# Kernel tuning notes

Hardware: AMD Instinct MI355X
Metric: run time of the kernel (lower is better)

Reference implementation:

```python
import jax, jax.numpy as jnp
import numpy as np

H = 32        # num query heads
HKV = 8       # num kv heads
D = 128       # head_dim
SCALE = D ** -0.5
FP8_MAX = 448.0   # e4m3 max
EPS = 1e-8
PAGE = 256
NPAGES = 20
SQ = 1024     # new diffusion tokens
CTX = 3072    # cached context tokens
DIFF_BLK = 32 # diffusion block size


def setup_inputs() -> dict:
    key = jax.random.key(0)
    ks = jax.random.split(key, 6)
    q = jax.random.normal(ks[0], (SQ, H * D), dtype=jnp.float32)
    k = jax.random.normal(ks[1], (SQ, HKV * D), dtype=jnp.float32)
    v = jax.random.normal(ks[2], (SQ, HKV * D), dtype=jnp.float32)
    # paged caches (values already stored in quantized units)
    k_cache = jax.random.normal(ks[3], (NPAGES, PAGE, HKV, D), dtype=jnp.float32)
    v_cache = jax.random.normal(ks[4], (NPAGES, PAGE, HKV, D), dtype=jnp.float32)
    # new tokens go into slots right after the context
    slot_mapping = jnp.arange(CTX, CTX + SQ, dtype=jnp.int32)
    cache_slots = jnp.arange(CTX, dtype=jnp.int32)
    # diffusion mask: full visibility of context, block-causal among new tokens
    blk = jnp.arange(SQ) // DIFF_BLK
    ctx_mask = jnp.ones((SQ, CTX), dtype=bool)
    new_mask = blk[:, None] >= blk[None, :]
    block_mask = jnp.concatenate([ctx_mask, new_mask], axis=1)  # [SQ, CTX+SQ]
    return {"q": q, "k": k, "v": v, "k_cache": k_cache, "v_cache": v_cache,
            "slot_mapping": slot_mapping, "cache_slots": cache_slots,
            "block_mask": block_mask}


def reference(q, k, v, k_cache, v_cache, slot_mapping, cache_slots, block_mask):
    k3 = k.reshape(-1, HKV, D)
    v3 = v.reshape(-1, HKV, D)
    qh = q.reshape(-1, H, D)

    # ---- FP8 scale tracking: per-kv-head absmax over (token, dim) ----
    k_scale = jnp.maximum(jnp.max(jnp.abs(k3), axis=(0, 2)) / FP8_MAX, EPS)  # [HKV]
    v_scale = jnp.maximum(jnp.max(jnp.abs(v3), axis=(0, 2)) / FP8_MAX, EPS)

    # ---- paged KV-cache store with inline quantization ----
    kc = k_cache.reshape(-1, HKV, D)  # [NPAGES*PAGE, HKV, D]
    vc = v_cache.reshape(-1, HKV, D)
    k_q = jnp.clip(k3 / k_scale[None, :, None], -FP8_MAX, FP8_MAX)
    v_q = jnp.clip(v3 / v_scale[None, :, None], -FP8_MAX, FP8_MAX)
    kc = kc.at[slot_mapping].set(k_q)
    vc = vc.at[slot_mapping].set(v_q)

    # ---- load context tokens from cache and dequantize ----
    k_ctx = kc[cache_slots] * k_scale[None, :, None]  # [CTX, HKV, D]
    v_ctx = vc[cache_slots] * v_scale[None, :, None]
    k_comb = jnp.concatenate([k_ctx, k3], axis=0)  # [SKV, HKV, D]
    v_comb = jnp.concatenate([v_ctx, v3], axis=0)

    # ---- GQA flex attention with token-level block mask ----
    G = H // HKV
    k_g = jnp.repeat(k_comb, G, axis=1)  # [SKV, H, D]
    v_g = jnp.repeat(v_comb, G, axis=1)
    scores = jnp.einsum('qhd,khd->hqk', qh, k_g) * SCALE  # [H, SQ, SKV]
    scores = jnp.where(block_mask[None, :, :], scores, jnp.float32(-1e30))
    probs = jax.nn.softmax(scores, axis=-1)
    o = jnp.einsum('hqk,khd->qhd', probs, v_g)  # [SQ, H, D]
    return o.reshape(-1, H * D)
```

## Files before the change

kernel.cpp:

```cpp
#include <hip/hip_runtime.h>
#include <stdint.h>

#define H 32
#define HKV 8
#define D 128
#define SQ 1024
#define CTX 3072
#define SKV 4096
#define FP8_MAX_C 448.0f
#define EPS_C 1e-8f

typedef __attribute__((ext_vector_type(4))) float f32x4;
typedef __attribute__((ext_vector_type(8))) __bf16 bf16x8;
typedef __attribute__((ext_vector_type(8))) unsigned short u16x8;

__device__ __forceinline__ unsigned short f2bf(float x) {
  unsigned int u = __builtin_bit_cast(unsigned int, x);
  u += 0x7fffu + ((u >> 16) & 1u);
  return (unsigned short)(u >> 16);
}

__device__ __forceinline__ f32x4 mfma16(bf16x8 a, bf16x8 b, f32x4 c) {
  return __builtin_amdgcn_mfma_f32_16x16x32_bf16(a, b, c, 0, 0, 0);
}

__device__ __forceinline__ void gld16(const unsigned short* g, char* l) {
  __builtin_amdgcn_global_load_lds(
      (const __attribute__((address_space(1))) unsigned int*)g,
      (__attribute__((address_space(3))) unsigned int*)l, 16, 0, 0);
}

__device__ __forceinline__ void stage_sync() {
  asm volatile("s_waitcnt vmcnt(0)" ::: "memory");
  __builtin_amdgcn_sched_barrier(0);
  __syncthreads();
}

__global__ void scales_part(const float* __restrict__ k,
                            const float* __restrict__ v,
                            unsigned int* __restrict__ smax) {
  const int b = blockIdx.x & 15;
  const int part = blockIdx.x >> 4;
  const float* src = (b < HKV) ? k : v;
  const int h = b & 7;
  const int tid = threadIdx.x;
  const int d0 = (tid & 31) * 4;
  float mx = 0.f;
  const int t1 = part * 128 + 128;
  for (int t = part * 128 + (tid >> 5); t < t1; t += 8) {
    float4 vv = *reinterpret_cast<const float4*>(src + (size_t)t * (HKV * D) + h * D + d0);
    mx = fmaxf(mx, fmaxf(fmaxf(fabsf(vv.x), fabsf(vv.y)),
                         fmaxf(fabsf(vv.z), fabsf(vv.w))));
  }
  __shared__ float red[256];
  red[tid] = mx;
  __syncthreads();
  for (int s = 128; s > 0; s >>= 1) {
    if (tid < s) red[tid] = fmaxf(red[tid], red[tid + s]);
    __syncthreads();
  }
  if (tid == 0) atomicMax(&smax[b], __float_as_uint(red[0]));
}

__global__ void scales_fin(const unsigned int* __restrict__ smax,
                           float* __restrict__ scales) {
  const int i = threadIdx.x;
  if (i < 16) scales[i] = fmaxf(__uint_as_float(smax[i]) / FP8_MAX_C, EPS_C);
}

__global__ void prep_kv(const float* __restrict__ k,
                        const float* __restrict__ v,
                        const float* __restrict__ k_cache,
                        const float* __restrict__ v_cache,
                        const int* __restrict__ cache_slots,
                        const float* __restrict__ scales,
                        unsigned short* __restrict__ k_comb,
                        unsigned short* __restrict__ v_combT) {
  if (blockIdx.x < 2048) {
    const int tid = blockIdx.x * 256 + threadIdx.x;
    const int d8 = tid & 15;
    const int t = (tid >> 4) & (SKV - 1);
    const int h = tid >> 16;
    const int d0 = d8 * 8;
    const float* src;
    float mul;
    if (t < CTX) {
      int slot = cache_slots[t];
      src = k_cache + (size_t)slot * (HKV * D) + h * D + d0;
      mul = scales[h];
    } else {
      src = k + (size_t)(t - CTX) * (HKV * D) + h * D + d0;
      mul = 1.f;
    }
    float4 a = *reinterpret_cast<const float4*>(src);
    float4 bb = *reinterpret_cast<const float4*>(src + 4);
    u16x8 r;
    r[0] = f2bf(a.x * mul);  r[1] = f2bf(a.y * mul);
    r[2] = f2bf(a.z * mul);  r[3] = f2bf(a.w * mul);
    r[4] = f2bf(bb.x * mul); r[5] = f2bf(bb.y * mul);
    r[6] = f2bf(bb.z * mul); r[7] = f2bf(bb.w * mul);
    *reinterpret_cast<u16x8*>(k_comb + ((size_t)h * SKV + t) * D + d0) = r;
  } else {
    const int tid = (blockIdx.x - 2048) * 256 + threadIdx.x;
    const int d = tid & 127;
    const int t8 = (tid >> 7) & 511;
    const int h = tid >> 16;
    const int t0 = t8 * 8;
    const float sc = scales[8 + h];
    u16x8 r;
#pragma unroll
    for (int i = 0; i < 8; ++i) {
      int t = t0 + i;
      float val;
      if (t < CTX) {
        int slot = cache_slots[t];
        val = v_cache[(size_t)slot * (HKV * D) + h * D + d] * sc;
      } else {
        val = v[(size_t)(t - CTX) * (HKV * D) + h * D + d];
      }
      r[i] = f2bf(val);
    }
    *reinterpret_cast<u16x8*>(v_combT + ((size_t)h * D + d) * SKV + t0) = r;
  }
}

#define LDBF(p) (*reinterpret_cast<const bf16x8*>(p))
#define Z4 ((f32x4){0.f, 0.f, 0.f, 0.f})

#define EXP4(SREG, P, RSV)                                                     \
  {                                                                            \
    P[0] = __builtin_amdgcn_exp2f(SREG[0] - m);                                \
    P[1] = __builtin_amdgcn_exp2f(SREG[1] - m);                                \
    P[2] = __builtin_amdgcn_exp2f(SREG[2] - m);                                \
    P[3] = __builtin_amdgcn_exp2f(SREG[3] - m);                                \
    RSV += (P[0] + P[1]) + (P[2] + P[3]);                                      \
  }

#define CVTPK(DST, LO, HI)                                                     \
  asm("v_cvt_pk_bf16_f32 %0, %1, %2" : "=v"(DST) : "v"(LO), "v"(HI));
#define SW32(A, B)                                                             \
  asm("v_permlane32_swap_b32 %0, %1" : "+v"(A), "+v"(B));
#define SW16(A, B)                                                             \
  asm("v_permlane16_swap_b32 %0, %1" : "+v"(A), "+v"(B));

#define PTRANS32(P0, P1, PF)                                                   \
  {                                                                            \
    unsigned int A_, Ap_, B_, Bp_;                                             \
    CVTPK(A_, P0[0], P0[1]) CVTPK(Ap_, P0[2], P0[3])                           \
    CVTPK(B_, P1[0], P1[1]) CVTPK(Bp_, P1[2], P1[3])                           \
    SW32(A_, B_) SW16(A_, B_)                                                  \
    SW32(Ap_, Bp_) SW16(Ap_, Bp_)                                              \
    union { unsigned int d[4]; bf16x8 v; } u_;                                 \
    u_.d[0] = A_; u_.d[1] = Ap_; u_.d[2] = B_; u_.d[3] = Bp_;                  \
    PF = u_.v;                                                                 \
  }

#define QKSF(SF, SA, SB)                                                       \
  {                                                                            \
    bf16x8 a0 = LDBF(kc + SF * 4096 + kx0);                                    \
    bf16x8 a1 = LDBF(kc + SF * 4096 + kx1);                                    \
    bf16x8 a2 = LDBF(kc + SF * 4096 + kx2);                                    \
    bf16x8 a3 = LDBF(kc + SF * 4096 + kx3);                                    \
    SA = mfma16(a0, qa0, SA); SA = mfma16(a1, qa1, SA);                        \
    SA = mfma16(a2, qa2, SA); SA = mfma16(a3, qa3, SA);                        \
    SB = mfma16(a0, qb0, SB); SB = mfma16(a1, qb1, SB);                        \
    SB = mfma16(a2, qb2, SB); SB = mfma16(a3, qb3, SB);                        \
  }

#define QLOADS                                                                 \
  {                                                                            \
    const float qs = 0.088388347648318447f * 1.4426950408889634f;              \
    const float* qpA = q + (size_t)(qbase + lo) * (H * D) + hqa * D;           \
    const float* qpB = qpA + D;                                                \
    _Pragma("unroll")                                                          \
    for (int ks = 0; ks < 4; ++ks) {                                           \
      float4 a = *reinterpret_cast<const float4*>(qpA + ks * 32 + g * 8);      \
      float4 b = *reinterpret_cast<const float4*>(qpA + ks * 32 + g * 8 + 4);  \
      union { unsigned short u[8]; bf16x8 v; } f;                              \
      f.u[0] = f2bf(a.x * qs); f.u[1] = f2bf(a.y * qs);                        \
      f.u[2] = f2bf(a.z * qs); f.u[3] = f2bf(a.w * qs);                        \
      f.u[4] = f2bf(b.x * qs); f.u[5] = f2bf(b.y * qs);                        \
      f.u[6] = f2bf(b.z * qs); f.u[7] = f2bf(b.w * qs);                        \
      if (ks == 0) qa0 = f.v; else if (ks == 1) qa1 = f.v;                     \
      else if (ks == 2) qa2 = f.v; else qa3 = f.v;                             \
      a = *reinterpret_cast<const float4*>(qpB + ks * 32 + g * 8);             \
      b = *reinterpret_cast<const float4*>(qpB + ks * 32 + g * 8 + 4);         \
      f.u[0] = f2bf(a.x * qs); f.u[1] = f2bf(a.y * qs);                        \
      f.u[2] = f2bf(a.z * qs); f.u[3] = f2bf(a.w * qs);                        \
      f.u[4] = f2bf(b.x * qs); f.u[5] = f2bf(b.y * qs);                        \
      f.u[6] = f2bf(b.z * qs); f.u[7] = f2bf(b.w * qs);                        \
      if (ks == 0) qb0 = f.v; else if (ks == 1) qb1 = f.v;                     \
      else if (ks == 2) qb2 = f.v; else qb3 = f.v;                             \
    }                                                                          \
  }

#define EPILOGUE(DSTEXPR)                                                      \
  lsa += __shfl_xor(lsa, 16); lsa += __shfl_xor(lsa, 32);                      \
  lsb += __shfl_xor(lsb, 16); lsb += __shfl_xor(lsb, 32);                      \
  float* dst = (DSTEXPR);                                                      \
  if (g == 0) {                                                                \
    float2 v;                                                                  \
    v.x = m; v.y = lsa;                                                        \
    *reinterpret_cast<float2*>(ml + ((size_t)part * SQ * H + (qbase + lo) * H + hqa) * 2) = v; \
    v.y = lsb;                                                                 \
    *reinterpret_cast<float2*>(ml + ((size_t)part * SQ * H + (qbase + lo) * H + hqa + 1) * 2) = v; \
  }                                                                            \
  _Pragma("unroll")                                                            \
  for (int r = 0; r < 4; ++r) {                                                \
    float* opa = dst + (size_t)(qbase + g * 4 + r) * (H * D) + hqa * D + lo;   \
    float* opb = opa + D;                                                      \
    opa[0 * 16] = aa0[r]; opb[0 * 16] = ab0[r];                                \
    opa[1 * 16] = aa1[r]; opb[1 * 16] = ab1[r];                                \
    opa[2 * 16] = aa2[r]; opb[2 * 16] = ab2[r];                                \
    opa[3 * 16] = aa3[r]; opb[3 * 16] = ab3[r];                                \
    opa[4 * 16] = aa4[r]; opb[4 * 16] = ab4[r];                                \
    opa[5 * 16] = aa5[r]; opb[5 * 16] = ab5[r];                                \
    opa[6 * 16] = aa6[r]; opb[6 * 16] = ab6[r];                                \
    opa[7 * 16] = aa7[r]; opb[7 * 16] = ab7[r];                                \
  }

#define RESCALE_ALL                                                            \
  if (!__all(pmax - m <= 8.f)) {                                               \
    float rm = fmaxf(pmax, __shfl_xor(pmax, 16));                              \
    rm = fmaxf(rm, __shfl_xor(rm, 32));                                        \
    float mn = fmaxf(m, rm);                                                   \
    float scl = __builtin_amdgcn_exp2f(m - mn);                                \
    lsa *= scl; lsb *= scl;                                                    \
    aa0 *= scl; aa1 *= scl; aa2 *= scl; aa3 *= scl;                            \
    aa4 *= scl; aa5 *= scl; aa6 *= scl; aa7 *= scl;                            \
    ab0 *= scl; ab1 *= scl; ab2 *= scl; ab3 *= scl;                            \
    ab4 *= scl; ab5 *= scl; ab6 *= scl; ab7 *= scl;                            \
    m = mn;                                                                    \
  }

#define STAGE32(TB, BUFO)                                                      \
  {                                                                            \
    _Pragma("unroll")                                                          \
    for (int j = 0; j < 2; ++j) {                                              \
      const int c = j * 256 + tid;                                             \
      const int r_ = c >> 4;                                                   \
      const int lc_ = (c & 15) ^ (r_ & 7);                                     \
      gld16(kb + (size_t)((TB) + r_) * D + lc_ * 8,                            \
            smem + (BUFO) + c * 16);                                           \
      const int dv_ = c >> 2;                                                  \
      const int cv_ = (c & 3) ^ ((dv_ >> 1) & 3);                              \
      gld16(vb + (size_t)dv_ * SKV + (TB) + cv_ * 8,                           \
            smem + (BUFO) + 8192 + c * 16);                                    \
    }                                                                          \
  }

#define SOFTMAX32                                                              \
  float pmax = fmaxf(fmaxf(fmaxf(sa0[0], sa0[1]), fmaxf(sa0[2], sa0[3])),      \
                     fmaxf(fmaxf(sa1[0], sa1[1]), fmaxf(sa1[2], sa1[3])));     \
  pmax = fmaxf(pmax,                                                           \
               fmaxf(fmaxf(fmaxf(sb0[0], sb0[1]), fmaxf(sb0[2], sb0[3])),      \
                     fmaxf(fmaxf(sb1[0], sb1[1]), fmaxf(sb1[2], sb1[3]))));    \
  RESCALE_ALL                                                                  \
  float pa0[4], pa1[4], pb0[4], pb1[4];                                        \
  EXP4(sa0, pa0, lsa) EXP4(sa1, pa1, lsa)                                      \
  EXP4(sb0, pb0, lsb) EXP4(sb1, pb1, lsb)                                      \
  PTRANS32(pa0, pa1, pfa)                                                      \
  PTRANS32(pb0, pb1, pfb)

#define VLOAD                                                                  \
  vf0 = LDBF(vc + 0 * 1024 + vx); vf1 = LDBF(vc + 1 * 1024 + vx);              \
  vf2 = LDBF(vc + 2 * 1024 + vx); vf3 = LDBF(vc + 3 * 1024 + vx);              \
  vf4 = LDBF(vc + 4 * 1024 + vx); vf5 = LDBF(vc + 5 * 1024 + vx);              \
  vf6 = LDBF(vc + 6 * 1024 + vx); vf7 = LDBF(vc + 7 * 1024 + vx);

#define PVREG                                                                  \
  aa0 = mfma16(pfa_p, vf0, aa0); ab0 = mfma16(pfb_p, vf0, ab0);                \
  aa1 = mfma16(pfa_p, vf1, aa1); ab1 = mfma16(pfb_p, vf1, ab1);                \
  aa2 = mfma16(pfa_p, vf2, aa2); ab2 = mfma16(pfb_p, vf2, ab2);                \
  aa3 = mfma16(pfa_p, vf3, aa3); ab3 = mfma16(pfb_p, vf3, ab3);                \
  aa4 = mfma16(pfa_p, vf4, aa4); ab4 = mfma16(pfb_p, vf4, ab4);                \
  aa5 = mfma16(pfa_p, vf5, aa5); ab5 = mfma16(pfb_p, vf5, ab5);                \
  aa6 = mfma16(pfa_p, vf6, aa6); ab6 = mfma16(pfb_p, vf6, ab6);                \
  aa7 = mfma16(pfa_p, vf7, aa7); ab7 = mfma16(pfb_p, vf7, ab7);

__launch_bounds__(256, 2)
__global__ void attn_kernel(const float* __restrict__ q,
                            const unsigned short* __restrict__ k_comb,
                            const unsigned short* __restrict__ v_combT,
                            float* __restrict__ out,
                            float* __restrict__ parts,
                            float* __restrict__ ml) {
  extern __shared__ __align__(16) char smem[];
  const int bid = blockIdx.x;
  const int hkv = bid & 7;
  const int qp_raw = (bid >> 3) & 31;
  const int part = bid >> 8;
  const int qp = part ? (31 - qp_raw) : qp_raw;
  const int tid = threadIdx.x;
  const int wid = tid >> 6;
  const int l = tid & 63;
  const int lo = l & 15;
  const int g = l >> 4;
  const int qbase = qp * 32 + (wid >> 1) * 16;
  const int hqa = hkv * 4 + (wid & 1) * 2;
  const int n32 = 97 + qp;
  const int t0 = (part * n32) >> 1;
  const int t1 = ((part + 1) * n32) >> 1;

  const unsigned short* kb = k_comb + (size_t)hkv * SKV * D;
  const unsigned short* vb = v_combT + (size_t)hkv * D * SKV;

  bf16x8 qa0, qa1, qa2, qa3, qb0, qb1, qb2, qb3;
  QLOADS

  f32x4 aa0 = Z4, aa1 = Z4, aa2 = Z4, aa3 = Z4;
  f32x4 aa4 = Z4, aa5 = Z4, aa6 = Z4, aa7 = Z4;
  f32x4 ab0 = Z4, ab1 = Z4, ab2 = Z4, ab3 = Z4;
  f32x4 ab4 = Z4, ab5 = Z4, ab6 = Z4, ab7 = Z4;
  float m = -1e30f;
  float lsa = 0.f, lsb = 0.f;

  const int xr = lo & 7;
  const int kx0 = ((0 + g) ^ xr) << 4;
  const int kx1 = ((4 + g) ^ xr) << 4;
  const int kx2 = ((8 + g) ^ xr) << 4;
  const int kx3 = ((12 + g) ^ xr) << 4;
  const int vx = ((g ^ ((lo >> 1) & 3))) << 4;
  const char* kbl = smem + lo * 256;
  const char* vbl = smem + 8192 + lo * 64;

  bf16x8 pfa_p, pfb_p;
  bf16x8 vf0, vf1, vf2, vf3, vf4, vf5, vf6, vf7;

  int cur = 0;
  STAGE32(t0 * 32, 0)
  stage_sync();

  {
    if (t0 + 1 < t1) STAGE32((t0 + 1) * 32, 16384)
    const char* kc = kbl;
    const char* vc = vbl;
    f32x4 sa0 = Z4, sa1 = Z4, sb0 = Z4, sb1 = Z4;
    __builtin_amdgcn_s_setprio(1);
    QKSF(0, sa0, sb0)
    QKSF(1, sa1, sb1)
    __builtin_amdgcn_s_setprio(0);
    bf16x8 pfa, pfb;
    SOFTMAX32
    VLOAD
    pfa_p = pfa; pfb_p = pfb;
    stage_sync();
    cur = 1;
  }

  for (int t = t0 + 1; t < t1; ++t) {
    if (t + 1 < t1) STAGE32((t + 1) * 32, (cur ^ 1) * 16384)

    const char* kc = kbl + cur * 16384;
    const char* vc = vbl + cur * 16384;

    f32x4 sa0 = Z4, sa1 = Z4, sb0 = Z4, sb1 = Z4;
    __builtin_amdgcn_s_setprio(1);
    QKSF(0, sa0, sb0)
    QKSF(1, sa1, sb1)
    PVREG
    __builtin_amdgcn_s_setprio(0);

    bf16x8 pfa, pfb;
    SOFTMAX32
    VLOAD
    pfa_p = pfa; pfb_p = pfb;

    stage_sync();
    cur ^= 1;
  }

  PVREG

  EPILOGUE(part == 0 ? out : parts)
}

__global__ void merge_kernel(float* __restrict__ out,
                             const float* __restrict__ parts,
                             const float* __restrict__ ml) {
  const int idx = blockIdx.x * 256 + threadIdx.x;
  const int h = (idx >> 5) & 31;
  const int qrow = idx >> 10;
  const float2* mp = (const float2*)ml;
  float2 A = mp[qrow * H + h];
  float2 B = mp[SQ * H + qrow * H + h];
  float mm = fmaxf(A.x, B.x);
  float wa = __builtin_amdgcn_exp2f(A.x - mm);
  float wb = __builtin_amdgcn_exp2f(B.x - mm);
  float inv = 1.f / (A.y * wa + B.y * wb);
  float4 oa = reinterpret_cast<float4*>(out)[idx];
  float4 ob = reinterpret_cast<const float4*>(parts)[idx];
  float4 r;
  r.x = (oa.x * wa + ob.x * wb) * inv;
  r.y = (oa.y * wa + ob.y * wb) * inv;
  r.z = (oa.z * wa + ob.z * wb) * inv;
  r.w = (oa.w * wa + ob.w * wb) * inv;
  reinterpret_cast<float4*>(out)[idx] = r;
}

extern "C" void kernel_launch(void* const* d_in, const int* in_sizes, int n_in,
                              void* d_out, int out_size, void* d_ws, size_t ws_size,
                              hipStream_t stream) {
  (void)in_sizes; (void)n_in; (void)out_size; (void)ws_size;
  const float* q = (const float*)d_in[0];
  const float* k = (const float*)d_in[1];
  const float* v = (const float*)d_in[2];
  const float* k_cache = (const float*)d_in[3];
  const float* v_cache = (const float*)d_in[4];
  const int* cache_slots = (const int*)d_in[6];
  float* out = (float*)d_out;

  unsigned int* smax = (unsigned int*)d_ws;
  float* scales = (float*)((char*)d_ws + 64);
  unsigned short* k_comb = (unsigned short*)((char*)d_ws + 256);
  unsigned short* v_combT = k_comb + (size_t)HKV * SKV * D;
  float* parts = (float*)((char*)d_ws + 256 + (size_t)16 * 1024 * 1024);
  float* ml = parts + (size_t)SQ * H * D;

  hipMemsetAsync(smax, 0, 64, stream);
  scales_part<<<128, 256, 0, stream>>>(k, v, smax);
  scales_fin<<<1, 64, 0, stream>>>(smax, scales);
  prep_kv<<<4096, 256, 0, stream>>>(k, v, k_cache, v_cache, cache_slots,
                                    scales, k_comb, v_combT);
  attn_kernel<<<512, 256, 32768, stream>>>(q, k_comb, v_combT, out, parts, ml);
  merge_kernel<<<4096, 256, 0, stream>>>(out, parts, ml);
}
```

Before: 110.9 us.

## Fuse FP8 scale reduction into KV prep and apply dequant scales in attention

Removes the separate scale-reduction and scale-finalize kernels by computing per-head absmax inside prep_kv while it already reads the new K/V tokens. Because scales are not known during prep, context K/V are stored unscaled in bf16 and the attention kernel applies the K scale to the scores and the V scale to the probabilities for context tiles (t < 96). This saves two launches and a redundant pass over K/V, at the cost of extra multiplies in the softmax path. Storing unscaled context values in bf16 also changes rounding slightly.

```diff
diff --git a/kernel.cpp b/kernel.cpp
--- a/kernel.cpp
+++ b/kernel.cpp
@@ -36,46 +36,17 @@
   __syncthreads();
 }
 
-__global__ void scales_part(const float* __restrict__ k,
-                            const float* __restrict__ v,
-                            unsigned int* __restrict__ smax) {
-  const int b = blockIdx.x & 15;
-  const int part = blockIdx.x >> 4;
-  const float* src = (b < HKV) ? k : v;
-  const int h = b & 7;
-  const int tid = threadIdx.x;
-  const int d0 = (tid & 31) * 4;
-  float mx = 0.f;
-  const int t1 = part * 128 + 128;
-  for (int t = part * 128 + (tid >> 5); t < t1; t += 8) {
-    float4 vv = *reinterpret_cast<const float4*>(src + (size_t)t * (HKV * D) + h * D + d0);
-    mx = fmaxf(mx, fmaxf(fmaxf(fabsf(vv.x), fabsf(vv.y)),
-                         fmaxf(fabsf(vv.z), fabsf(vv.w))));
-  }
-  __shared__ float red[256];
-  red[tid] = mx;
-  __syncthreads();
-  for (int s = 128; s > 0; s >>= 1) {
-    if (tid < s) red[tid] = fmaxf(red[tid], red[tid + s]);
-    __syncthreads();
-  }
-  if (tid == 0) atomicMax(&smax[b], __float_as_uint(red[0]));
-}
-
-__global__ void scales_fin(const unsigned int* __restrict__ smax,
-                           float* __restrict__ scales) {
-  const int i = threadIdx.x;
-  if (i < 16) scales[i] = fmaxf(__uint_as_float(smax[i]) / FP8_MAX_C, EPS_C);
-}
-
 __global__ void prep_kv(const float* __restrict__ k,
                         const float* __restrict__ v,
                         const float* __restrict__ k_cache,
                         const float* __restrict__ v_cache,
                         const int* __restrict__ cache_slots,
-                        const float* __restrict__ scales,
                         unsigned short* __restrict__ k_comb,
-                        unsigned short* __restrict__ v_combT) {
+                        unsigned short* __restrict__ v_combT,
+                        unsigned int* __restrict__ smax) {
+  __shared__ float red[256];
+  float mx = 0.f;
+  int sidx = -1;
   if (blockIdx.x < 2048) {
     const int tid = blockIdx.x * 256 + threadIdx.x;
     const int d8 = tid & 15;
@@ -83,57 +54,74 @@
     const int h = tid >> 16;
     const int d0 = d8 * 8;
     const float* src;
-    float mul;
     if (t < CTX) {
       int slot = cache_slots[t];
       src = k_cache + (size_t)slot * (HKV * D) + h * D + d0;
-      mul = scales[h];
     } else {
       src = k + (size_t)(t - CTX) * (HKV * D) + h * D + d0;
-      mul = 1.f;
+      sidx = h;
     }
     float4 a = *reinterpret_cast<const float4*>(src);
     float4 bb = *reinterpret_cast<const float4*>(src + 4);
     u16x8 r;
-    r[0] = f2bf(a.x * mul);  r[1] = f2bf(a.y * mul);
-    r[2] = f2bf(a.z * mul);  r[3] = f2bf(a.w * mul);
-    r[4] = f2bf(bb.x * mul); r[5] = f2bf(bb.y * mul);
-    r[6] = f2bf(bb.z * mul); r[7] = f2bf(bb.w * mul);
+    r[0] = f2bf(a.x);  r[1] = f2bf(a.y);
+    r[2] = f2bf(a.z);  r[3] = f2bf(a.w);
+    r[4] = f2bf(bb.x); r[5] = f2bf(bb.y);
+    r[6] = f2bf(bb.z); r[7] = f2bf(bb.w);
     *reinterpret_cast<u16x8*>(k_comb + ((size_t)h * SKV + t) * D + d0) = r;
+    if (sidx >= 0) {
+      mx = fmaxf(fmaxf(fmaxf(fabsf(a.x), fabsf(a.y)),
+                       fmaxf(fabsf(a.z), fabsf(a.w))),
+                 fmaxf(fmaxf(fabsf(bb.x), fabsf(bb.y)),
+                       fmaxf(fabsf(bb.z), fabsf(bb.w))));
+    }
   } else {
     const int tid = (blockIdx.x - 2048) * 256 + threadIdx.x;
     const int d = tid & 127;
     const int t8 = (tid >> 7) & 511;
     const int h = tid >> 16;
     const int t0 = t8 * 8;
-    const float sc = scales[8 + h];
     u16x8 r;
+    if (t0 < CTX) {
 #pragma unroll
-    for (int i = 0; i < 8; ++i) {
-      int t = t0 + i;
-      float val;
-      if (t < CTX) {
-        int slot = cache_slots[t];
-        val = v_cache[(size_t)slot * (HKV * D) + h * D + d] * sc;
-      } else {
-        val = v[(size_t)(t - CTX) * (HKV * D) + h * D + d];
+      for (int i = 0; i < 8; ++i) {
+        int slot = cache_slots[t0 + i];
+        r[i] = f2bf(v_cache[(size_t)slot * (HKV * D) + h * D + d]);
       }
-      r[i] = f2bf(val);
+    } else {
+      sidx = 8 + h;
+#pragma unroll
+      for (int i = 0; i < 8; ++i) {
+        float val = v[(size_t)(t0 + i - CTX) * (HKV * D) + h * D + d];
+        mx = fmaxf(mx, fabsf(val));
+        r[i] = f2bf(val);
+      }
     }
     *reinterpret_cast<u16x8*>(v_combT + ((size_t)h * D + d) * SKV + t0) = r;
   }
+  if (sidx >= 0) {
+    const int tx = threadIdx.x;
+    red[tx] = mx;
+    __syncthreads();
+    for (int s = 128; s > 0; s >>= 1) {
+      if (tx < s) red[tx] = fmaxf(red[tx], red[tx + s]);
+      __syncthreads();
+    }
+    if (tx == 0) atomicMax(&smax[sidx], __float_as_uint(red[0]));
+  }
 }
 
 #define LDBF(p) (*reinterpret_cast<const bf16x8*>(p))
 #define Z4 ((f32x4){0.f, 0.f, 0.f, 0.f})
 
-#define EXP4(SREG, P, RSV)                                                     \
+#define EXP4(SREG, P, RSV, VS)                                                 \
   {                                                                            \
     P[0] = __builtin_amdgcn_exp2f(SREG[0] - m);                                \
     P[1] = __builtin_amdgcn_exp2f(SREG[1] - m);                                \
     P[2] = __builtin_amdgcn_exp2f(SREG[2] - m);                                \
     P[3] = __builtin_amdgcn_exp2f(SREG[3] - m);                                \
     RSV += (P[0] + P[1]) + (P[2] + P[3]);                                      \
+    P[0] *= VS; P[1] *= VS; P[2] *= VS; P[3] *= VS;                            \
   }
 
 #define CVTPK(DST, LO, HI)                                                     \
@@ -173,24 +161,24 @@
     const float* qpA = q + (size_t)(qbase + lo) * (H * D) + hqa * D;           \
     const float* qpB = qpA + D;                                                \
     _Pragma("unroll")                                                          \
-    for (int ks = 0; ks < 4; ++ks) {                                           \
-      float4 a = *reinterpret_cast<const float4*>(qpA + ks * 32 + g * 8);      \
-      float4 b = *reinterpret_cast<const float4*>(qpA + ks * 32 + g * 8 + 4);  \
+    for (int ks_ = 0; ks_ < 4; ++ks_) {                                        \
+      float4 a = *reinterpret_cast<const float4*>(qpA + ks_ * 32 + g * 8);     \
+      float4 b = *reinterpret_cast<const float4*>(qpA + ks_ * 32 + g * 8 + 4); \
       union { unsigned short u[8]; bf16x8 v; } f;                              \
       f.u[0] = f2bf(a.x * qs); f.u[1] = f2bf(a.y * qs);                        \
       f.u[2] = f2bf(a.z * qs); f.u[3] = f2bf(a.w * qs);                        \
       f.u[4] = f2bf(b.x * qs); f.u[5] = f2bf(b.y * qs);                        \
       f.u[6] = f2bf(b.z * qs); f.u[7] = f2bf(b.w * qs);                        \
-      if (ks == 0) qa0 = f.v; else if (ks == 1) qa1 = f.v;                     \
-      else if (ks == 2) qa2 = f.v; else qa3 = f.v;                             \
-      a = *reinterpret_cast<const float4*>(qpB + ks * 32 + g * 8);             \
-      b = *reinterpret_cast<const float4*>(qpB + ks * 32 + g * 8 + 4);         \
+      if (ks_ == 0) qa0 = f.v; else if (ks_ == 1) qa1 = f.v;                   \
+      else if (ks_ == 2) qa2 = f.v; else qa3 = f.v;                            \
+      a = *reinterpret_cast<const float4*>(qpB + ks_ * 32 + g * 8);            \
+      b = *reinterpret_cast<const float4*>(qpB + ks_ * 32 + g * 8 + 4);        \
       f.u[0] = f2bf(a.x * qs); f.u[1] = f2bf(a.y * qs);                        \
       f.u[2] = f2bf(a.z * qs); f.u[3] = f2bf(a.w * qs);                        \
       f.u[4] = f2bf(b.x * qs); f.u[5] = f2bf(b.y * qs);                        \
       f.u[6] = f2bf(b.z * qs); f.u[7] = f2bf(b.w * qs);                        \
-      if (ks == 0) qb0 = f.v; else if (ks == 1) qb1 = f.v;                     \
-      else if (ks == 2) qb2 = f.v; else qb3 = f.v;                             \
+      if (ks_ == 0) qb0 = f.v; else if (ks_ == 1) qb1 = f.v;                   \
+      else if (ks_ == 2) qb2 = f.v; else qb3 = f.v;                            \
     }                                                                          \
   }
 
@@ -249,7 +237,8 @@
     }                                                                          \
   }
 
-#define SOFTMAX32                                                              \
+#define SOFTMAX32(KSEL, VSEL)                                                  \
+  sa0 *= (KSEL); sa1 *= (KSEL); sb0 *= (KSEL); sb1 *= (KSEL);                  \
   float pmax = fmaxf(fmaxf(fmaxf(sa0[0], sa0[1]), fmaxf(sa0[2], sa0[3])),      \
                      fmaxf(fmaxf(sa1[0], sa1[1]), fmaxf(sa1[2], sa1[3])));     \
   pmax = fmaxf(pmax,                                                           \
@@ -257,8 +246,8 @@
                      fmaxf(fmaxf(sb1[0], sb1[1]), fmaxf(sb1[2], sb1[3]))));    \
   RESCALE_ALL                                                                  \
   float pa0[4], pa1[4], pb0[4], pb1[4];                                        \
-  EXP4(sa0, pa0, lsa) EXP4(sa1, pa1, lsa)                                      \
-  EXP4(sb0, pb0, lsb) EXP4(sb1, pb1, lsb)                                      \
+  EXP4(sa0, pa0, lsa, (VSEL)) EXP4(sa1, pa1, lsa, (VSEL))                      \
+  EXP4(sb0, pb0, lsb, (VSEL)) EXP4(sb1, pb1, lsb, (VSEL))                      \
   PTRANS32(pa0, pa1, pfa)                                                      \
   PTRANS32(pb0, pb1, pfb)
 
@@ -282,6 +271,7 @@
 __global__ void attn_kernel(const float* __restrict__ q,
                             const unsigned short* __restrict__ k_comb,
                             const unsigned short* __restrict__ v_combT,
+                            const unsigned int* __restrict__ smax,
                             float* __restrict__ out,
                             float* __restrict__ parts,
                             float* __restrict__ ml) {
@@ -302,6 +292,9 @@
   const int t0 = (part * n32) >> 1;
   const int t1 = ((part + 1) * n32) >> 1;
 
+  const float kscale = fmaxf(__uint_as_float(smax[hkv]) / FP8_MAX_C, EPS_C);
+  const float vscale = fmaxf(__uint_as_float(smax[8 + hkv]) / FP8_MAX_C, EPS_C);
+
   const unsigned short* kb = k_comb + (size_t)hkv * SKV * D;
   const unsigned short* vb = v_combT + (size_t)hkv * D * SKV;
 
@@ -341,7 +334,9 @@
     QKSF(1, sa1, sb1)
     __builtin_amdgcn_s_setprio(0);
     bf16x8 pfa, pfb;
-    SOFTMAX32
+    const float ksel = (t0 < 96) ? kscale : 1.f;
+    const float vsel = (t0 < 96) ? vscale : 1.f;
+    SOFTMAX32(ksel, vsel)
     VLOAD
     pfa_p = pfa; pfb_p = pfb;
     stage_sync();
@@ -362,7 +357,9 @@
     __builtin_amdgcn_s_setprio(0);
 
     bf16x8 pfa, pfb;
-    SOFTMAX32
+    const float ksel = (t < 96) ? kscale : 1.f;
+    const float vsel = (t < 96) ? vscale : 1.f;
+    SOFTMAX32(ksel, vsel)
     VLOAD
     pfa_p = pfa; pfb_p = pfb;
 
@@ -411,17 +408,15 @@
   float* out = (float*)d_out;
 
   unsigned int* smax = (unsigned int*)d_ws;
-  float* scales = (float*)((char*)d_ws + 64);
   unsigned short* k_comb = (unsigned short*)((char*)d_ws + 256);
   unsigned short* v_combT = k_comb + (size_t)HKV * SKV * D;
   float* parts = (float*)((char*)d_ws + 256 + (size_t)16 * 1024 * 1024);
   float* ml = parts + (size_t)SQ * H * D;
 
   hipMemsetAsync(smax, 0, 64, stream);
-  scales_part<<<128, 256, 0, stream>>>(k, v, smax);
-  scales_fin<<<1, 64, 0, stream>>>(smax, scales);
   prep_kv<<<4096, 256, 0, stream>>>(k, v, k_cache, v_cache, cache_slots,
-                                    scales, k_comb, v_combT);
-  attn_kernel<<<512, 256, 32768, stream>>>(q, k_comb, v_combT, out, parts, ml);
+                                    k_comb, v_combT, smax);
+  attn_kernel<<<512, 256, 32768, stream>>>(q, k_comb, v_combT, smax, out,
+                                           parts, ml);
   merge_kernel<<<4096, 256, 0, stream>>>(out, parts, ml);
 }
```

New measurement: 109.1 us (median of 2 runs). No clear change (-1.7%).
